# Kernel tuning notes

Measured on AMD Instinct MI355X. Metric: run time of the kernel, lower is better.

The kernel has to match this reference:

```python
import jax, jax.numpy as jnp
import numpy as np

NUM_CAPSULE = 16
DIM_CAPSULE = 32
ROUTINGS = 4
EPS = 1e-07


def squash(x, axis=-1):
    # NOTE: faithful to the source: x / sqrt(sum(x^2) + eps) (unit-norm style),
    # NOT the standard Hinton squash.
    s2 = jnp.sum(x * x, axis=axis, keepdims=True)
    return x / jnp.sqrt(s2 + EPS)


def setup_inputs() -> dict:
    key = jax.random.key(0)
    k1, k2 = jax.random.split(key)
    B, N_in, D_in = 128, 1024, 256
    x = jax.random.normal(k1, (B, N_in, D_in), dtype=jnp.float32)
    # xavier_normal over (1, D_in, NUM_CAPSULE*DIM_CAPSULE)
    fan_in, fan_out = D_in, NUM_CAPSULE * DIM_CAPSULE
    std = np.sqrt(2.0 / (fan_in + fan_out))
    W = jax.random.normal(k2, (1, D_in, NUM_CAPSULE * DIM_CAPSULE), dtype=jnp.float32) * std
    return {"x": x, "W": W}


def reference(x, W):
    B, N_in, _ = x.shape
    # u_hat: [B, N_in, num_cap*dim_cap] -> [B, num_cap, N_in, dim_cap]
    u_hat = jnp.matmul(x, W[0])
    u_hat = u_hat.reshape(B, N_in, NUM_CAPSULE, DIM_CAPSULE).transpose(0, 2, 1, 3)

    b = jnp.zeros((B, NUM_CAPSULE, N_in), dtype=u_hat.dtype)
    outputs = None
    for i in range(ROUTINGS):
        # torch permutes to softmax over the num_capsule axis; equivalent to axis=1 here
        c = jax.nn.softmax(b, axis=1)                      # [B, num_cap, N_in]
        outputs = squash(jnp.einsum('bij,bijk->bik', c, u_hat))  # [B, num_cap, dim_cap]
        if i < ROUTINGS - 1:
            b = jnp.einsum('bik,bijk->bij', outputs, u_hat)
    return outputs
```

## Files before the change

kernel.cpp:

```cpp
#include <hip/hip_runtime.h>
#include <hip/hip_bf16.h>

typedef unsigned int u32;
typedef float f32x4 __attribute__((ext_vector_type(4)));
typedef __bf16 bf16x8 __attribute__((ext_vector_type(8)));

#define BATCH 128
#define NIN   1024
#define DIN   256
#define NC    16
#define DC    32
#define NCOL  512

__device__ __forceinline__ float bflo(u32 v){ return __uint_as_float(v << 16); }
__device__ __forceinline__ float bfhi(u32 v){ return __uint_as_float(v & 0xffff0000u); }
__device__ __forceinline__ u32 bfround(u32 ua){ return (ua + 0x7fffu + ((ua >> 16) & 1u)) >> 16; }
__device__ __forceinline__ u32 pack2(float a, float b){
    return (bfround(__float_as_uint(a)) & 0xffffu) | (bfround(__float_as_uint(b)) << 16);
}
__device__ __forceinline__ bf16x8 ldfrag(const u32* p){
    return __builtin_bit_cast(bf16x8, *(const uint4*)p);
}
__device__ __forceinline__ int rot4(int n){ return (n + (n >> 3) + (n >> 5)) & 3; }

__global__ __launch_bounds__(256) void k_wconv(const float* __restrict__ W, uint4* __restrict__ Wt2){
    int id = blockIdx.x * 256 + threadIdx.x;
    int l = id & 63, ks = (id >> 6) & 7, ntile = id >> 9;
    int n = ntile * 16 + (l & 15);
    int w0 = ks * 16 + (l >> 4) * 4;
    u32 r[4];
    #pragma unroll
    for (int e = 0; e < 4; e++){
        int w = w0 + e;
        r[e] = pack2(W[(size_t)(2 * w) * NCOL + n], W[(size_t)(2 * w + 1) * NCOL + n]);
    }
    Wt2[id] = make_uint4(r[0], r[1], r[2], r[3]);
}

__global__ __launch_bounds__(512) void k_gemm(const float* __restrict__ x, const uint4* __restrict__ Wt2,
                                              u32* __restrict__ uhat, float* __restrict__ yp0){
    __shared__ __align__(16) u32 xl[64 * 128];
    const int t = threadIdx.x, jb = blockIdx.x, b = blockIdx.y;
    const int lane = t & 63, wv = t >> 6;
    const int l15 = lane & 15, q = lane >> 4;

    uint4 bnx[4], bc[4];
    #pragma unroll
    for (int nt = 0; nt < 4; nt++)
        bnx[nt] = Wt2[(size_t)(((wv * 4 + nt) * 8 + 0) * 64) + lane];

    {
        const float4* xg = (const float4*)(x + ((size_t)b * NIN + jb * 64) * DIN);
        #pragma unroll
        for (int m = 0; m < 4; m++){
            int p = t + 512 * m;
            float4 a = xg[2 * p], c = xg[2 * p + 1];
            int j = p >> 5, wq = 4 * (p & 31);
            uint4 v;
            v.x = pack2(a.x, a.y); v.y = pack2(a.z, a.w);
            v.z = pack2(c.x, c.y); v.w = pack2(c.z, c.w);
            *(uint4*)&xl[j * 128 + ((wq + 4 * j) & 127)] = v;
        }
    }
    __syncthreads();

    f32x4 acc[4][4];
    #pragma unroll
    for (int mt = 0; mt < 4; mt++)
        #pragma unroll
        for (int nt = 0; nt < 4; nt++) acc[mt][nt] = (f32x4){0.f, 0.f, 0.f, 0.f};
    #pragma unroll
    for (int ks = 0; ks < 8; ks++){
        bf16x8 af[4];
        #pragma unroll
        for (int mt = 0; mt < 4; mt++){
            int jr = mt * 16 + l15;
            af[mt] = ldfrag(&xl[jr * 128 + ((ks * 16 + q * 4 + 4 * jr) & 127)]);
        }
        #pragma unroll
        for (int nt = 0; nt < 4; nt++) bc[nt] = bnx[nt];
        if (ks < 7){
            #pragma unroll
            for (int nt = 0; nt < 4; nt++)
                bnx[nt] = Wt2[(size_t)(((wv * 4 + nt) * 8 + ks + 1) * 64) + lane];
        }
        #pragma unroll
        for (int mt = 0; mt < 4; mt++)
            #pragma unroll
            for (int nt = 0; nt < 4; nt++)
                acc[mt][nt] = __builtin_amdgcn_mfma_f32_16x16x32_bf16(af[mt], __builtin_bit_cast(bf16x8, bc[nt]), acc[mt][nt], 0, 0, 0);
    }

    #pragma unroll
    for (int nt = 0; nt < 4; nt++){
        float v = 0.f;
        #pragma unroll
        for (int mt = 0; mt < 4; mt++)
            #pragma unroll
            for (int r = 0; r < 4; r++) v += acc[mt][nt][r];
        v += __shfl_xor(v, 16);
        v += __shfl_xor(v, 32);
        if (lane < 16)
            yp0[((size_t)jb * BATCH + b) * NCOL + wv * 64 + nt * 16 + lane] = v;
    }

    u32* ub = uhat + (size_t)b * 32 * NCOL * 16;
    #pragma unroll
    for (int nt = 0; nt < 4; nt++){
        int n = wv * 64 + nt * 16 + l15;
        #pragma unroll
        for (int mt = 0; mt < 4; mt++){
            int jp = mt * 8 + q * 2;
            int ch = jb * 2 + (jp >> 4);
            int wp = jp & 15;
            uint2 v;
            v.x = pack2(acc[mt][nt][0], acc[mt][nt][1]);
            v.y = pack2(acc[mt][nt][2], acc[mt][nt][3]);
            *(uint2*)&ub[((size_t)ch * NCOL + n) * 16 + wp] = v;
        }
    }
}

__global__ __launch_bounds__(256) void k_route(const u32* __restrict__ uhat, const float* __restrict__ og,
                                               float* __restrict__ yp){
    __shared__ __align__(16) u32 ul[NCOL * 16];
    __shared__ float ol[NCOL];
    __shared__ float bbc[NC * 33];
    const int ch = blockIdx.x, b = blockIdx.y, t = threadIdx.x;

    ol[t] = og[b * NCOL + t];
    ol[t + 256] = og[b * NCOL + t + 256];
    {
        const uint4* ug = (const uint4*)(uhat + ((size_t)b * 32 + ch) * NCOL * 16);
        uint4* ul4 = (uint4*)ul;
        #pragma unroll
        for (int m = 0; m < 8; m++){
            int id = t + 256 * m;
            int n = id >> 2, s = id & 3;
            ul4[n * 4 + ((s + rot4(n)) & 3)] = ug[id];
        }
    }
    __syncthreads();

    {
        int i = t >> 4, jq = t & 15;
        float oc[DC];
        #pragma unroll
        for (int e = 0; e < 8; e++) *(float4*)&oc[4 * e] = *(const float4*)&ol[i * DC + 4 * e];
        float a0 = 0.f, a1 = 0.f;
        #pragma unroll
        for (int k = 0; k < DC; k++){
            int n = i * DC + k;
            u32 v = ul[n * 16 + ((jq + 4 * rot4(n)) & 15)];
            a0 += oc[k] * bflo(v);
            a1 += oc[k] * bfhi(v);
        }
        bbc[i * 33 + 2 * jq]     = a0;
        bbc[i * 33 + 2 * jq + 1] = a1;
    }
    __syncthreads();

    if (t < 32){
        float m = -1e30f;
        #pragma unroll
        for (int i = 0; i < NC; i++) m = fmaxf(m, bbc[i * 33 + t]);
        float s = 0.f;
        #pragma unroll
        for (int i = 0; i < NC; i++){ float e = __expf(bbc[i * 33 + t] - m); bbc[i * 33 + t] = e; s += e; }
        float inv = 1.f / s;
        #pragma unroll
        for (int i = 0; i < NC; i++) bbc[i * 33 + t] *= inv;
    }
    __syncthreads();

    #pragma unroll
    for (int h = 0; h < 2; h++){
        int n = t + 256 * h;
        int i = n >> 5;
        float cc[32];
        #pragma unroll
        for (int j = 0; j < 32; j++) cc[j] = bbc[i * 33 + j];
        float s = 0.f;
        const uint4* ul4 = (const uint4*)ul;
        #pragma unroll
        for (int s4 = 0; s4 < 4; s4++){
            uint4 v = ul4[n * 4 + ((s4 + rot4(n)) & 3)];
            int j0 = s4 * 8;
            s += cc[j0+0] * bflo(v.x) + cc[j0+1] * bfhi(v.x)
               + cc[j0+2] * bflo(v.y) + cc[j0+3] * bfhi(v.y)
               + cc[j0+4] * bflo(v.z) + cc[j0+5] * bfhi(v.z)
               + cc[j0+6] * bflo(v.w) + cc[j0+7] * bfhi(v.w);
        }
        yp[((size_t)ch * BATCH + b) * NCOL + n] = s;
    }
}

__global__ __launch_bounds__(512) void k_sz(const float* __restrict__ yp, int P,
                                            float* __restrict__ og, float* __restrict__ out, int final){
    const int b = blockIdx.x, t = threadIdx.x;
    float s = 0.f;
    for (int p = 0; p < P; p++) s += yp[((size_t)p * BATCH + b) * NCOL + t];
    float v = s * s;
    v += __shfl_xor(v, 1); v += __shfl_xor(v, 2); v += __shfl_xor(v, 4);
    v += __shfl_xor(v, 8); v += __shfl_xor(v, 16);
    float o = s / sqrtf(v + 1e-7f);
    og[b * NCOL + t] = o;
    if (final) out[(size_t)b * NCOL + t] = o;
}

extern "C" void kernel_launch(void* const* d_in, const int* in_sizes, int n_in,
                              void* d_out, int out_size, void* d_ws, size_t ws_size,
                              hipStream_t stream){
    const float* x = (const float*)d_in[0];
    const float* W = (const float*)d_in[1];
    float* out = (float*)d_out;
    float* f = (float*)d_ws;
    float* og   = f;
    float* yp0  = f + 65536;
    float* ypr  = f + 65536 + 1048576;
    uint4* Wt2  = (uint4*)(f + 65536 + 1048576 + 2097152);
    u32*   uhat = (u32*)(f + 65536 + 1048576 + 2097152 + 65536);

    k_wconv<<<64, 256, 0, stream>>>(W, Wt2);
    k_gemm<<<dim3(16, BATCH), 512, 0, stream>>>(x, Wt2, uhat, yp0);
    k_sz<<<BATCH, 512, 0, stream>>>(yp0, 16, og, out, 0);
    for (int it = 1; it < 4; it++){
        k_route<<<dim3(32, BATCH), 256, 0, stream>>>(uhat, og, ypr);
        k_sz<<<BATCH, 512, 0, stream>>>(ypr, 32, og, out, it == 3 ? 1 : 0);
    }
}
```

Before: 340.8 us.

## Make gemm and route blocks persistent over several chunks with double-buffered prefetch

k_gemm and k_route now each process TPB=4 chunks per block, using double-buffered shared memory so the global loads for the next chunk overlap compute on the current one. The gemm tile shrinks to 32 rows, which cuts per-block accumulator registers. k_sz is split across 4 blocks per batch with 128 threads to raise parallelism. The cost is a quarter as many blocks and doubled LDS per block, which may reduce occupancy and latency hiding across the grid.

```diff
diff --git a/kernel.cpp b/kernel.cpp
--- a/kernel.cpp
+++ b/kernel.cpp
@@ -11,6 +11,9 @@
 #define NC    16
 #define DC    32
 #define NCOL  512
+#define JT    32
+#define NCH   32
+#define TPB   4
 
 __device__ __forceinline__ float bflo(u32 v){ return __uint_as_float(v << 16); }
 __device__ __forceinline__ float bfhi(u32 v){ return __uint_as_float(v & 0xffff0000u); }
@@ -38,174 +41,221 @@
 }
 
 __global__ __launch_bounds__(512) void k_gemm(const float* __restrict__ x, const uint4* __restrict__ Wt2,
-                                              u32* __restrict__ uhat, float* __restrict__ yp0){
-    __shared__ __align__(16) u32 xl[64 * 128];
-    const int t = threadIdx.x, jb = blockIdx.x, b = blockIdx.y;
+                                              u32* __restrict__ uhat, float* __restrict__ yp){
+    __shared__ __align__(16) u32 xl[2][JT * 128];
+    const int t = threadIdx.x, bid = blockIdx.x;
     const int lane = t & 63, wv = t >> 6;
     const int l15 = lane & 15, q = lane >> 4;
-
-    uint4 bnx[4], bc[4];
-    #pragma unroll
-    for (int nt = 0; nt < 4; nt++)
-        bnx[nt] = Wt2[(size_t)(((wv * 4 + nt) * 8 + 0) * 64) + lane];
-
+    const int b = (bid * TPB) >> 5;
+    const int ch0 = (bid * TPB) & 31;
+    const float4* xg = (const float4*)(x + (size_t)b * NIN * DIN);
+
+    float4 pf[4];
     {
-        const float4* xg = (const float4*)(x + ((size_t)b * NIN + jb * 64) * DIN);
-        #pragma unroll
-        for (int m = 0; m < 4; m++){
+        int base = (ch0 * JT * DIN) >> 2;
+        #pragma unroll
+        for (int m = 0; m < 2; m++){
+            pf[2*m]   = xg[base + 2 * (t + 512 * m)];
+            pf[2*m+1] = xg[base + 2 * (t + 512 * m) + 1];
+        }
+        #pragma unroll
+        for (int m = 0; m < 2; m++){
             int p = t + 512 * m;
-            float4 a = xg[2 * p], c = xg[2 * p + 1];
             int j = p >> 5, wq = 4 * (p & 31);
             uint4 v;
-            v.x = pack2(a.x, a.y); v.y = pack2(a.z, a.w);
-            v.z = pack2(c.x, c.y); v.w = pack2(c.z, c.w);
-            *(uint4*)&xl[j * 128 + ((wq + 4 * j) & 127)] = v;
+            v.x = pack2(pf[2*m].x, pf[2*m].y);   v.y = pack2(pf[2*m].z, pf[2*m].w);
+            v.z = pack2(pf[2*m+1].x, pf[2*m+1].y); v.w = pack2(pf[2*m+1].z, pf[2*m+1].w);
+            *(uint4*)&xl[0][j * 128 + ((wq + 4 * j) & 127)] = v;
         }
     }
     __syncthreads();
 
-    f32x4 acc[4][4];
-    #pragma unroll
-    for (int mt = 0; mt < 4; mt++)
-        #pragma unroll
-        for (int nt = 0; nt < 4; nt++) acc[mt][nt] = (f32x4){0.f, 0.f, 0.f, 0.f};
-    #pragma unroll
-    for (int ks = 0; ks < 8; ks++){
-        bf16x8 af[4];
-        #pragma unroll
-        for (int mt = 0; mt < 4; mt++){
-            int jr = mt * 16 + l15;
-            af[mt] = ldfrag(&xl[jr * 128 + ((ks * 16 + q * 4 + 4 * jr) & 127)]);
-        }
-        #pragma unroll
-        for (int nt = 0; nt < 4; nt++) bc[nt] = bnx[nt];
-        if (ks < 7){
-            #pragma unroll
-            for (int nt = 0; nt < 4; nt++)
-                bnx[nt] = Wt2[(size_t)(((wv * 4 + nt) * 8 + ks + 1) * 64) + lane];
-        }
-        #pragma unroll
-        for (int mt = 0; mt < 4; mt++)
-            #pragma unroll
-            for (int nt = 0; nt < 4; nt++)
-                acc[mt][nt] = __builtin_amdgcn_mfma_f32_16x16x32_bf16(af[mt], __builtin_bit_cast(bf16x8, bc[nt]), acc[mt][nt], 0, 0, 0);
-    }
-
-    #pragma unroll
-    for (int nt = 0; nt < 4; nt++){
-        float v = 0.f;
-        #pragma unroll
-        for (int mt = 0; mt < 4; mt++)
-            #pragma unroll
-            for (int r = 0; r < 4; r++) v += acc[mt][nt][r];
-        v += __shfl_xor(v, 16);
-        v += __shfl_xor(v, 32);
-        if (lane < 16)
-            yp0[((size_t)jb * BATCH + b) * NCOL + wv * 64 + nt * 16 + lane] = v;
-    }
-
-    u32* ub = uhat + (size_t)b * 32 * NCOL * 16;
-    #pragma unroll
-    for (int nt = 0; nt < 4; nt++){
-        int n = wv * 64 + nt * 16 + l15;
-        #pragma unroll
-        for (int mt = 0; mt < 4; mt++){
-            int jp = mt * 8 + q * 2;
-            int ch = jb * 2 + (jp >> 4);
-            int wp = jp & 15;
-            uint2 v;
-            v.x = pack2(acc[mt][nt][0], acc[mt][nt][1]);
-            v.y = pack2(acc[mt][nt][2], acc[mt][nt][3]);
-            *(uint2*)&ub[((size_t)ch * NCOL + n) * 16 + wp] = v;
-        }
+    for (int tl = 0; tl < TPB; tl++){
+        const int ch = ch0 + tl, buf = tl & 1;
+        if (tl + 1 < TPB){
+            int base = ((ch + 1) * JT * DIN) >> 2;
+            #pragma unroll
+            for (int m = 0; m < 2; m++){
+                pf[2*m]   = xg[base + 2 * (t + 512 * m)];
+                pf[2*m+1] = xg[base + 2 * (t + 512 * m) + 1];
+            }
+        }
+        f32x4 acc[2][4];
+        #pragma unroll
+        for (int mt = 0; mt < 2; mt++)
+            #pragma unroll
+            for (int nt = 0; nt < 4; nt++) acc[mt][nt] = (f32x4){0.f,0.f,0.f,0.f};
+        uint4 bnx[4], bcr[4];
+        #pragma unroll
+        for (int nt = 0; nt < 4; nt++) bnx[nt] = Wt2[(size_t)(((wv*4+nt)*8) * 64) + lane];
+        #pragma unroll
+        for (int ks = 0; ks < 8; ks++){
+            bf16x8 af[2];
+            #pragma unroll
+            for (int mt = 0; mt < 2; mt++){
+                int jr = mt * 16 + l15;
+                af[mt] = ldfrag(&xl[buf][jr * 128 + ((ks * 16 + q * 4 + 4 * jr) & 127)]);
+            }
+            #pragma unroll
+            for (int nt = 0; nt < 4; nt++) bcr[nt] = bnx[nt];
+            if (ks < 7){
+                #pragma unroll
+                for (int nt = 0; nt < 4; nt++)
+                    bnx[nt] = Wt2[(size_t)(((wv*4+nt)*8 + ks + 1) * 64) + lane];
+            }
+            #pragma unroll
+            for (int mt = 0; mt < 2; mt++)
+                #pragma unroll
+                for (int nt = 0; nt < 4; nt++)
+                    acc[mt][nt] = __builtin_amdgcn_mfma_f32_16x16x32_bf16(af[mt], __builtin_bit_cast(bf16x8, bcr[nt]), acc[mt][nt], 0, 0, 0);
+        }
+        #pragma unroll
+        for (int nt = 0; nt < 4; nt++){
+            float v = 0.f;
+            #pragma unroll
+            for (int mt = 0; mt < 2; mt++)
+                #pragma unroll
+                for (int r = 0; r < 4; r++) v += acc[mt][nt][r];
+            v += __shfl_xor(v, 16);
+            v += __shfl_xor(v, 32);
+            if (lane < 16)
+                yp[((size_t)ch * BATCH + b) * NCOL + wv * 64 + nt * 16 + lane] = v;
+        }
+        u32* ub = uhat + ((size_t)(b * NCH + ch) * NCOL) * 16;
+        #pragma unroll
+        for (int nt = 0; nt < 4; nt++){
+            int n = wv * 64 + nt * 16 + l15;
+            #pragma unroll
+            for (int mt = 0; mt < 2; mt++){
+                uint2 v;
+                v.x = pack2(acc[mt][nt][0], acc[mt][nt][1]);
+                v.y = pack2(acc[mt][nt][2], acc[mt][nt][3]);
+                *(uint2*)&ub[n * 16 + mt * 8 + q * 2] = v;
+            }
+        }
+        if (tl + 1 < TPB){
+            #pragma unroll
+            for (int m = 0; m < 2; m++){
+                int p = t + 512 * m;
+                int j = p >> 5, wq = 4 * (p & 31);
+                uint4 v;
+                v.x = pack2(pf[2*m].x, pf[2*m].y);   v.y = pack2(pf[2*m].z, pf[2*m].w);
+                v.z = pack2(pf[2*m+1].x, pf[2*m+1].y); v.w = pack2(pf[2*m+1].z, pf[2*m+1].w);
+                *(uint4*)&xl[buf ^ 1][j * 128 + ((wq + 4 * j) & 127)] = v;
+            }
+        }
+        __syncthreads();
     }
 }
 
 __global__ __launch_bounds__(256) void k_route(const u32* __restrict__ uhat, const float* __restrict__ og,
                                                float* __restrict__ yp){
-    __shared__ __align__(16) u32 ul[NCOL * 16];
+    __shared__ __align__(16) u32 ul[2][NCOL * 16];
     __shared__ float ol[NCOL];
     __shared__ float bbc[NC * 33];
-    const int ch = blockIdx.x, b = blockIdx.y, t = threadIdx.x;
+    const int t = threadIdx.x, bid = blockIdx.x;
+    const int b = (bid * TPB) >> 5;
+    const int ch0 = (bid * TPB) & 31;
 
     ol[t] = og[b * NCOL + t];
     ol[t + 256] = og[b * NCOL + t + 256];
+
+    uint4 pf[8];
+    const uint4* ug = (const uint4*)(uhat + ((size_t)b * NCH) * NCOL * 16);
     {
-        const uint4* ug = (const uint4*)(uhat + ((size_t)b * 32 + ch) * NCOL * 16);
-        uint4* ul4 = (uint4*)ul;
+        #pragma unroll
+        for (int m = 0; m < 8; m++) pf[m] = ug[(size_t)ch0 * 2048 + t + 256 * m];
+        uint4* ul4 = (uint4*)ul[0];
         #pragma unroll
         for (int m = 0; m < 8; m++){
             int id = t + 256 * m;
             int n = id >> 2, s = id & 3;
-            ul4[n * 4 + ((s + rot4(n)) & 3)] = ug[id];
+            ul4[n * 4 + ((s + rot4(n)) & 3)] = pf[m];
         }
     }
     __syncthreads();
 
-    {
-        int i = t >> 4, jq = t & 15;
-        float oc[DC];
-        #pragma unroll
-        for (int e = 0; e < 8; e++) *(float4*)&oc[4 * e] = *(const float4*)&ol[i * DC + 4 * e];
-        float a0 = 0.f, a1 = 0.f;
-        #pragma unroll
-        for (int k = 0; k < DC; k++){
-            int n = i * DC + k;
-            u32 v = ul[n * 16 + ((jq + 4 * rot4(n)) & 15)];
-            a0 += oc[k] * bflo(v);
-            a1 += oc[k] * bfhi(v);
-        }
-        bbc[i * 33 + 2 * jq]     = a0;
-        bbc[i * 33 + 2 * jq + 1] = a1;
-    }
-    __syncthreads();
-
-    if (t < 32){
-        float m = -1e30f;
-        #pragma unroll
-        for (int i = 0; i < NC; i++) m = fmaxf(m, bbc[i * 33 + t]);
-        float s = 0.f;
-        #pragma unroll
-        for (int i = 0; i < NC; i++){ float e = __expf(bbc[i * 33 + t] - m); bbc[i * 33 + t] = e; s += e; }
-        float inv = 1.f / s;
-        #pragma unroll
-        for (int i = 0; i < NC; i++) bbc[i * 33 + t] *= inv;
-    }
-    __syncthreads();
-
-    #pragma unroll
-    for (int h = 0; h < 2; h++){
-        int n = t + 256 * h;
-        int i = n >> 5;
-        float cc[32];
-        #pragma unroll
-        for (int j = 0; j < 32; j++) cc[j] = bbc[i * 33 + j];
-        float s = 0.f;
-        const uint4* ul4 = (const uint4*)ul;
-        #pragma unroll
-        for (int s4 = 0; s4 < 4; s4++){
-            uint4 v = ul4[n * 4 + ((s4 + rot4(n)) & 3)];
-            int j0 = s4 * 8;
-            s += cc[j0+0] * bflo(v.x) + cc[j0+1] * bfhi(v.x)
-               + cc[j0+2] * bflo(v.y) + cc[j0+3] * bfhi(v.y)
-               + cc[j0+4] * bflo(v.z) + cc[j0+5] * bfhi(v.z)
-               + cc[j0+6] * bflo(v.w) + cc[j0+7] * bfhi(v.w);
-        }
-        yp[((size_t)ch * BATCH + b) * NCOL + n] = s;
-    }
-}
-
-__global__ __launch_bounds__(512) void k_sz(const float* __restrict__ yp, int P,
+    for (int tl = 0; tl < TPB; tl++){
+        const int ch = ch0 + tl, buf = tl & 1;
+        if (tl + 1 < TPB){
+            #pragma unroll
+            for (int m = 0; m < 8; m++) pf[m] = ug[(size_t)(ch + 1) * 2048 + t + 256 * m];
+        }
+        {
+            int i = t >> 4, jq = t & 15;
+            float oc[DC];
+            #pragma unroll
+            for (int e = 0; e < 8; e++) *(float4*)&oc[4 * e] = *(const float4*)&ol[i * DC + 4 * e];
+            float a0 = 0.f, a1 = 0.f;
+            #pragma unroll
+            for (int k = 0; k < DC; k++){
+                int n = i * DC + k;
+                u32 v = ul[buf][n * 16 + ((jq + 4 * rot4(n)) & 15)];
+                a0 += oc[k] * bflo(v);
+                a1 += oc[k] * bfhi(v);
+            }
+            bbc[i * 33 + 2 * jq]     = a0;
+            bbc[i * 33 + 2 * jq + 1] = a1;
+        }
+        __syncthreads();
+        if (t < 32){
+            float m = -1e30f;
+            #pragma unroll
+            for (int i = 0; i < NC; i++) m = fmaxf(m, bbc[i * 33 + t]);
+            float s = 0.f;
+            #pragma unroll
+            for (int i = 0; i < NC; i++){ float e = __expf(bbc[i * 33 + t] - m); bbc[i * 33 + t] = e; s += e; }
+            float inv = 1.f / s;
+            #pragma unroll
+            for (int i = 0; i < NC; i++) bbc[i * 33 + t] *= inv;
+        }
+        __syncthreads();
+        #pragma unroll
+        for (int h = 0; h < 2; h++){
+            int n = t + 256 * h;
+            int i = n >> 5;
+            float cc[32];
+            #pragma unroll
+            for (int j = 0; j < 32; j++) cc[j] = bbc[i * 33 + j];
+            float s = 0.f;
+            const uint4* ul4 = (const uint4*)ul[buf];
+            #pragma unroll
+            for (int s4 = 0; s4 < 4; s4++){
+                uint4 v = ul4[n * 4 + ((s4 + rot4(n)) & 3)];
+                int j0 = s4 * 8;
+                s += cc[j0+0] * bflo(v.x) + cc[j0+1] * bfhi(v.x)
+                   + cc[j0+2] * bflo(v.y) + cc[j0+3] * bfhi(v.y)
+                   + cc[j0+4] * bflo(v.z) + cc[j0+5] * bfhi(v.z)
+                   + cc[j0+6] * bflo(v.w) + cc[j0+7] * bfhi(v.w);
+            }
+            yp[((size_t)ch * BATCH + b) * NCOL + n] = s;
+        }
+        if (tl + 1 < TPB){
+            uint4* ul4 = (uint4*)ul[buf ^ 1];
+            #pragma unroll
+            for (int m = 0; m < 8; m++){
+                int id = t + 256 * m;
+                int n = id >> 2, s = id & 3;
+                ul4[n * 4 + ((s + rot4(n)) & 3)] = pf[m];
+            }
+        }
+        __syncthreads();
+    }
+}
+
+__global__ __launch_bounds__(128) void k_sz(const float* __restrict__ yp,
                                             float* __restrict__ og, float* __restrict__ out, int final){
-    const int b = blockIdx.x, t = threadIdx.x;
+    const int gx = blockIdx.x, b = blockIdx.y, t = threadIdx.x;
+    const int n = gx * 128 + t;
     float s = 0.f;
-    for (int p = 0; p < P; p++) s += yp[((size_t)p * BATCH + b) * NCOL + t];
+    #pragma unroll 8
+    for (int p = 0; p < NCH; p++) s += yp[((size_t)p * BATCH + b) * NCOL + n];
     float v = s * s;
     v += __shfl_xor(v, 1); v += __shfl_xor(v, 2); v += __shfl_xor(v, 4);
     v += __shfl_xor(v, 8); v += __shfl_xor(v, 16);
     float o = s / sqrtf(v + 1e-7f);
-    og[b * NCOL + t] = o;
-    if (final) out[(size_t)b * NCOL + t] = o;
+    og[b * NCOL + n] = o;
+    if (final) out[(size_t)b * NCOL + n] = o;
 }
 
 extern "C" void kernel_launch(void* const* d_in, const int* in_sizes, int n_in,
@@ -216,16 +266,15 @@
     float* out = (float*)d_out;
     float* f = (float*)d_ws;
     float* og   = f;
-    float* yp0  = f + 65536;
-    float* ypr  = f + 65536 + 1048576;
-    uint4* Wt2  = (uint4*)(f + 65536 + 1048576 + 2097152);
-    u32*   uhat = (u32*)(f + 65536 + 1048576 + 2097152 + 65536);
+    float* ypr  = f + 65536;
+    uint4* Wt2  = (uint4*)(f + 65536 + 2097152);
+    u32*   uhat = (u32*)(f + 65536 + 2097152 + 65536);
 
     k_wconv<<<64, 256, 0, stream>>>(W, Wt2);
-    k_gemm<<<dim3(16, BATCH), 512, 0, stream>>>(x, Wt2, uhat, yp0);
-    k_sz<<<BATCH, 512, 0, stream>>>(yp0, 16, og, out, 0);
+    k_gemm<<<(BATCH * NCH) / TPB, 512, 0, stream>>>(x, Wt2, uhat, ypr);
+    k_sz<<<dim3(4, BATCH), 128, 0, stream>>>(ypr, og, out, 0);
     for (int it = 1; it < 4; it++){
-        k_route<<<dim3(32, BATCH), 256, 0, stream>>>(uhat, og, ypr);
-        k_sz<<<BATCH, 512, 0, stream>>>(ypr, 32, og, out, it == 3 ? 1 : 0);
-    }
-}
+        k_route<<<(BATCH * NCH) / TPB, 256, 0, stream>>>(uhat, og, ypr);
+        k_sz<<<dim3(4, BATCH), 128, 0, stream>>>(ypr, og, out, it == 3 ? 1 : 0);
+    }
+}
```

Measured after the change: 423.5 us. +24.2%, slower.
